# Kernel optimization log

Measured on AMD Instinct MI355X. Metric: run time of the kernel, lower is better.

Reference implementation:

```python
import jax, jax.numpy as jnp
import numpy as np

IN_N, OUT_N, KER, FEAT, HID = 50, 10, 10, 66, 256
VLEN = KER + OUT_N            # 20
VSEQ = IN_N - KER - OUT_N + 1 # 31
IF = 2 * VLEN                 # 40, GCN input feature size
NBLK = 12                     # 6 GC blocks x 2 graph convs
BN_EPS = 1e-5


def get_dct_matrix(N):
    k = np.arange(N)[:, None]
    i = np.arange(N)[None, :]
    w = np.full((N, 1), np.sqrt(2.0 / N))
    w[0, 0] = np.sqrt(1.0 / N)
    dct = (w * np.cos(np.pi * (i + 0.5) * k / N)).astype(np.float32)
    idct = np.linalg.inv(dct).astype(np.float32)
    return jnp.array(dct), jnp.array(idct)


def conv1d(x, w, b):
    # x: [B, Cin, T], w: [Cout, Cin, K]
    y = jax.lax.conv_general_dilated(x, w, (1,), 'VALID',
                                     dimension_numbers=('NCH', 'OIH', 'NCH'))
    return y + b[None, :, None]


def _forward(x, q_w1, q_b1, q_w2, q_b2, k_w1, k_b1, k_w2, k_b2,
             gin_w, gin_att, gin_b, bn_in_g, bn_in_b,
             blk_w, blk_att, blk_b, blk_bn_g, blk_bn_b,
             gout_w, gout_att, gout_b):
    dct, idct = get_dct_matrix(VLEN)
    B = x.shape[0]
    x = x[:, :IN_N]
    # q/k conv nets (Conv1d k=6 -> ReLU -> Conv1d k=5 -> ReLU)
    qs = jnp.transpose(x[:, IN_N - OUT_N:], (0, 2, 1))   # [B, FEAT, OUT_N]
    ksrc = jnp.transpose(x[:, :IN_N - OUT_N], (0, 2, 1)) # [B, FEAT, IN_N-OUT_N]
    q = jax.nn.relu(conv1d(jax.nn.relu(conv1d(qs, q_w1, q_b1)), q_w2, q_b2))    # [B, HID, 1]
    k = jax.nn.relu(conv1d(jax.nn.relu(conv1d(ksrc, k_w1, k_b1)), k_w2, k_b2))  # [B, HID, VSEQ]
    scores = jnp.einsum('bhq,bhs->bqs', q, k)            # [B, 1, VSEQ]
    att = scores[:, 0, :] / jnp.sum(scores, axis=-1)     # sum-normalized, [B, VSEQ]
    # overlapping windowed value gather + DCT
    vidx = np.arange(VLEN)[None, :] + np.arange(VSEQ)[:, None]
    value_mat = x[:, vidx, :]                             # [B, VSEQ, VLEN, FEAT]
    value_dct = jnp.einsum('bslf,lm->bsfm', value_mat, dct)  # [B, VSEQ, FEAT, VLEN]
    vdct_r = value_dct.reshape(B, FEAT, VSEQ, VLEN)       # raw reshape, as in torch source
    att_final = jnp.einsum('bs,bfsl->bfl', att, vdct_r)   # [B, FEAT, VLEN]
    # padded query (last KER frames + OUT_N repeats of last frame) in DCT space
    pidx = np.concatenate([np.arange(IN_N - KER, IN_N), np.full(OUT_N, IN_N - 1)])
    padded_query = jnp.einsum('bfl,lm->bfm', jnp.transpose(x[:, pidx], (0, 2, 1)), dct)
    gcn_inp = jnp.concatenate([padded_query, att_final], axis=2)  # [B, FEAT, IF]

    def gc(h, w, a, b):  # graph conv with learnable adjacency over FEAT nodes
        return jnp.einsum('nm,bmf->bnf', a, h @ w) + b

    def bn(h, g, beta):  # eval-mode BatchNorm1d over flattened [FEAT*feat] dim
        hf = h.reshape(B, -1)
        return ((hf / jnp.sqrt(1.0 + BN_EPS)) * g + beta).reshape(h.shape)

    y = jnp.tanh(bn(gc(gcn_inp, gin_w, gin_att, gin_b), bn_in_g, bn_in_b))
    for i in range(0, NBLK, 2):
        res = y
        y = jnp.tanh(bn(gc(y, blk_w[i], blk_att[i], blk_b[i]), blk_bn_g[i], blk_bn_b[i]))
        y = jnp.tanh(bn(gc(y, blk_w[i + 1], blk_att[i + 1], blk_b[i + 1]), blk_bn_g[i + 1], blk_bn_b[i + 1]))
        y = y + res
    gcn_out = gc(y, gout_w, gout_att, gout_b) + gcn_inp   # [B, FEAT, IF]
    return jnp.einsum('bfl,lm->bfm', gcn_out[:, :, :VLEN], idct)  # [B, FEAT, VLEN]


def setup_inputs():
    key = jax.random.key(0)
    ks = jax.random.split(key, 12)
    B = 2048
    s = 0.05
    NN = FEAT * HID
    return {
        'x': jax.random.normal(ks[0], (B, IN_N, FEAT), jnp.float32),
        'q_w1': jax.random.normal(ks[1], (HID, FEAT, 6), jnp.float32) * s,
        'q_b1': jnp.zeros((HID,), jnp.float32),
        'q_w2': jax.random.normal(ks[2], (HID, HID, 5), jnp.float32) * s,
        'q_b2': jnp.zeros((HID,), jnp.float32),
        'k_w1': jax.random.normal(ks[3], (HID, FEAT, 6), jnp.float32) * s,
        'k_b1': jnp.zeros((HID,), jnp.float32),
        'k_w2': jax.random.normal(ks[4], (HID, HID, 5), jnp.float32) * s,
        'k_b2': jnp.zeros((HID,), jnp.float32),
        'gin_w': jax.random.normal(ks[5], (IF, HID), jnp.float32) * s,
        'gin_att': jax.random.normal(ks[6], (FEAT, FEAT), jnp.float32) * s,
        'gin_b': jnp.zeros((HID,), jnp.float32),
        'bn_in_g': jnp.ones((NN,), jnp.float32),
        'bn_in_b': jnp.zeros((NN,), jnp.float32),
        'blk_w': jax.random.normal(ks[7], (NBLK, HID, HID), jnp.float32) * s,
        'blk_att': jax.random.normal(ks[8], (NBLK, FEAT, FEAT), jnp.float32) * s,
        'blk_b': jnp.zeros((NBLK, HID), jnp.float32),
        'blk_bn_g': jnp.ones((NBLK, NN), jnp.float32),
        'blk_bn_b': jnp.zeros((NBLK, NN), jnp.float32),
        'gout_w': jax.random.normal(ks[9], (HID, IF), jnp.float32) * s,
        'gout_att': jax.random.normal(ks[10], (FEAT, FEAT), jnp.float32) * s,
        'gout_b': jnp.zeros((IF,), jnp.float32),
    }


def reference(x, q_w1, q_b1, q_w2, q_b2, k_w1, k_b1, k_w2, k_b2,
              gin_w, gin_att, gin_b, bn_in_g, bn_in_b,
              blk_w, blk_att, blk_b, blk_bn_g, blk_bn_b,
              gout_w, gout_att, gout_b):
    return _forward(x, q_w1, q_b1, q_w2, q_b2, k_w1, k_b1, k_w2, k_b2,
                    gin_w, gin_att, gin_b, bn_in_g, bn_in_b,
                    blk_w, blk_att, blk_b, blk_bn_g, blk_bn_b,
                    gout_w, gout_att, gout_b)
```

## Files before the change

### kernel.cpp

```cpp
#include <hip/hip_runtime.h>
#include <math.h>

typedef unsigned short u16;
typedef unsigned int u32;

#define FEATN 66
#define HIDN 256
#define NNDIM 16896
#define INVS 0.9999950000374998f
#ifndef M_PI
#define M_PI 3.14159265358979323846
#endif

typedef __attribute__((ext_vector_type(4))) float f32x4;
typedef __attribute__((ext_vector_type(2))) float f32x2;
typedef __attribute__((ext_vector_type(8))) short s16x8;

__device__ __forceinline__ u32 bf_rne(float x) {
    u32 i = __float_as_uint(x);
    return (i + 0x7fffu + ((i >> 16) & 1u)) >> 16;
}

__global__ void dct_kernel(float* __restrict__ dct) {
    int t = threadIdx.x;
    if (t < 400) {
        int k = t / 20, i = t % 20;
        double w = (k == 0) ? sqrt(1.0 / 20.0) : sqrt(2.0 / 20.0);
        dct[t] = (float)(w * cos(M_PI * (i + 0.5) * k / 20.0));
    }
}

__global__ __launch_bounds__(256) void pack_w_kernel(
    const float* __restrict__ blk_w, u16* __restrict__ wh, u16* __restrict__ wl) {
    int gid = blockIdx.x * 256 + threadIdx.x;
    if (gid >= 12 * 65536) return;
    int layer = gid >> 16, rmd = gid & 65535;
    int ks = rmd >> 13;
    int r2 = rmd & 8191;
    int ct = r2 >> 9;
    int r3 = r2 & 511;
    int lane = r3 >> 3, j = r3 & 7;
    int k = ks * 32 + (lane >> 4) * 8 + j;
    int n = ct * 16 + (lane & 15);
    float v = blk_w[(size_t)layer * 65536 + k * 256 + n];
    u32 rhi = bf_rne(v);
    float hif = __uint_as_float(rhi << 16);
    u32 rlo = bf_rne(v - hif);
    wh[gid] = (u16)rhi;
    wl[gid] = (u16)rlo;
}

__global__ __launch_bounds__(256) void pack_w2_kernel(
    const float* __restrict__ w2, u16* __restrict__ wh, u16* __restrict__ wl) {
    int gid = blockIdx.x * 256 + threadIdx.x;
    if (gid >= 40 * 16 * 512) return;
    int ks = gid >> 13;
    int r2 = gid & 8191;
    int ct = r2 >> 9;
    int r3 = r2 & 511;
    int lane = r3 >> 3, j = r3 & 7;
    int k = ks * 32 + (lane >> 4) * 8 + j;
    int n = ct * 16 + (lane & 15);
    int h = k & 255, t = k >> 8;
    float v = w2[(size_t)n * 1280 + h * 5 + t];
    u32 rhi = bf_rne(v);
    float hif = __uint_as_float(rhi << 16);
    u32 rlo = bf_rne(v - hif);
    wh[gid] = (u16)rhi;
    wl[gid] = (u16)rlo;
}

__global__ __launch_bounds__(256) void pack_w1_kernel(
    const float* __restrict__ w1, u16* __restrict__ wh, u16* __restrict__ wl) {
    int gid = blockIdx.x * 256 + threadIdx.x;
    if (gid >= 13 * 16 * 512) return;
    int ks = gid >> 13;
    int r2 = gid & 8191;
    int ct = r2 >> 9;
    int r3 = r2 & 511;
    int lane = r3 >> 3, j = r3 & 7;
    int k = ks * 32 + (lane >> 4) * 8 + j;
    int n = ct * 16 + (lane & 15);
    float v = 0.f;
    if (k < 396) {
        int f = k % 66, t = k / 66;
        v = w1[(size_t)n * 396 + f * 6 + t];
    }
    u32 rhi = bf_rne(v);
    float hif = __uint_as_float(rhi << 16);
    u32 rlo = bf_rne(v - hif);
    wh[gid] = (u16)rhi;
    wl[gid] = (u16)rlo;
}

__global__ __launch_bounds__(256) void pack_att_kernel(
    const float* __restrict__ blk_att, u16* __restrict__ ah, u16* __restrict__ al) {
    int gid = blockIdx.x * 256 + threadIdx.x;
    if (gid >= 12 * 7680) return;
    int layer = gid / 7680, rem = gid % 7680;
    int rt = rem / 1536, rem2 = rem % 1536;
    int ks = rem2 / 512, r3 = rem2 % 512;
    int lane = r3 >> 3, j = r3 & 7;
    int n = rt * 16 + (lane & 15);
    int k = ks * 32 + (lane >> 4) * 8 + j;
    float v = (n < 66 && k < 66) ? blk_att[(size_t)layer * 4356 + n * 66 + k] : 0.f;
    u32 rhi = bf_rne(v);
    float hif = __uint_as_float(rhi << 16);
    u32 rlo = bf_rne(v - hif);
    ah[gid] = (u16)rhi;
    al[gid] = (u16)rlo;
}

__global__ __launch_bounds__(256, 1) void conv1_mfma_kernel(
    const float* __restrict__ x,
    const u16* __restrict__ whq, const u16* __restrict__ wlq,
    const u16* __restrict__ whk, const u16* __restrict__ wlk,
    const float* __restrict__ bq, const float* __restrict__ bk,
    float* __restrict__ q1, float* __restrict__ k1, int Cc, int nbq) {
    __shared__ u16 Ah[64 * 136];
    __shared__ u16 Al[64 * 136];
    const int tid = threadIdx.x;
    const int lane = tid & 63, wid = tid >> 6;
    const int m = lane & 15, quad = lane >> 4;
    const bool isq = ((int)blockIdx.x < nbq);
    const int bid = isq ? (int)blockIdx.x : ((int)blockIdx.x - nbq);
    const int rows = isq ? Cc * 5 : Cc * 35;
    const int row0 = bid * 64;
    const u16* wh = isq ? whq : whk;
    const u16* wl = isq ? wlq : wlk;
    const float* bias = isq ? bq : bk;
    float* out = isq ? q1 : k1;

    const int cq = tid & 31;
    const int r0t = (tid >> 5) * 8;
    int rbc[8]; bool vld[8];
#pragma unroll
    for (int s = 0; s < 8; s++) {
        int grow = row0 + r0t + s;
        int rbv;
        if (isq) { int bb = grow / 5;  rbv = bb * 3300 + 2640 + (grow - bb * 5) * 66; }
        else     { int bb = grow / 35; rbv = bb * 3300 + (grow - bb * 35) * 66; }
        vld[s] = (grow < rows);
        rbc[s] = vld[s] ? rbv : 0;
    }

    f32x4 acc[4][4];
#pragma unroll
    for (int rt = 0; rt < 4; rt++)
#pragma unroll
        for (int ct = 0; ct < 4; ct++) acc[rt][ct] = (f32x4)0.f;

    f32x2 ldA[16], ldB[16];

    auto LOADP = [&](f32x2* dst, int ph) {
        const int off = ph * 128 + cq * 4;
        const bool kok = (off < 396);
        const int o = kok ? off : 0;
#pragma unroll
        for (int s = 0; s < 8; s++) {
            const float* p = x + rbc[s] + o;
            dst[2 * s]     = *(const f32x2*)p;
            dst[2 * s + 1] = *(const f32x2*)(p + 2);
        }
    };
    auto STOREP = [&](const f32x2* src, int ph) {
        const bool kok = (ph * 128 + cq * 4) < 396;
#pragma unroll
        for (int s = 0; s < 8; s++) {
            float v0 = src[2 * s][0], v1 = src[2 * s][1];
            float v2 = src[2 * s + 1][0], v3 = src[2 * s + 1][1];
            if (!vld[s] || !kok) { v0 = v1 = v2 = v3 = 0.f; }
            u32 H0 = bf_rne(v0), H1 = bf_rne(v1), H2 = bf_rne(v2), H3 = bf_rne(v3);
            u32 L0 = bf_rne(v0 - __uint_as_float(H0 << 16));
            u32 L1 = bf_rne(v1 - __uint_as_float(H1 << 16));
            u32 L2 = bf_rne(v2 - __uint_as_float(H2 << 16));
            u32 L3 = bf_rne(v3 - __uint_as_float(H3 << 16));
            int o = (r0t + s) * 136 + cq * 4;
            *(uint2*)&Ah[o] = make_uint2(H0 | (H1 << 16), H2 | (H3 << 16));
            *(uint2*)&Al[o] = make_uint2(L0 | (L1 << 16), L2 | (L3 << 16));
        }
    };
    auto MFMAP = [&](int ph) {
#pragma unroll
        for (int ks = 0; ks < 4; ks++) {
            const int ksg = ph * 4 + ks;
            if (ksg >= 13) break;
            s16x8 ahf[4], alf[4], bhf[4], blf[4];
#pragma unroll
            for (int rt = 0; rt < 4; rt++) {
                int o2 = (rt * 16 + m) * 136 + ks * 32 + quad * 8;
                ahf[rt] = *(const s16x8*)&Ah[o2];
                alf[rt] = *(const s16x8*)&Al[o2];
            }
#pragma unroll
            for (int ct = 0; ct < 4; ct++) {
                size_t boff = ((size_t)(ksg * 16 + wid * 4 + ct)) * 512 + lane * 8;
                bhf[ct] = *(const s16x8*)&wh[boff];
                blf[ct] = *(const s16x8*)&wl[boff];
            }
#pragma unroll
            for (int rt = 0; rt < 4; rt++) {
#pragma unroll
                for (int ct = 0; ct < 4; ct++) {
                    acc[rt][ct] = __builtin_amdgcn_mfma_f32_16x16x32_bf16(
                        ahf[rt], bhf[ct], acc[rt][ct], 0, 0, 0);
                    acc[rt][ct] = __builtin_amdgcn_mfma_f32_16x16x32_bf16(
                        ahf[rt], blf[ct], acc[rt][ct], 0, 0, 0);
                    acc[rt][ct] = __builtin_amdgcn_mfma_f32_16x16x32_bf16(
                        alf[rt], bhf[ct], acc[rt][ct], 0, 0, 0);
                }
            }
        }
    };

    LOADP(ldA, 0);
    for (int ph = 0; ph < 4; ph += 2) {
        __syncthreads();
        STOREP(ldA, ph);
        LOADP(ldB, ph + 1);
        __syncthreads();
        MFMAP(ph);
        __syncthreads();
        STOREP(ldB, ph + 1);
        if (ph + 2 < 4) LOADP(ldA, ph + 2);
        __syncthreads();
        MFMAP(ph + 1);
    }

#pragma unroll
    for (int rt = 0; rt < 4; rt++) {
        int rb2 = row0 + rt * 16 + quad * 4;
#pragma unroll
        for (int r = 0; r < 4; r++) {
            int grow = rb2 + r;
            if (grow >= rows) continue;
#pragma unroll
            for (int ct = 0; ct < 4; ct++) {
                int f = wid * 64 + ct * 16 + m;
                float v = acc[rt][ct][r] + bias[f];
                out[(size_t)grow * 256 + f] = fmaxf(v, 0.f);
            }
        }
    }
}

__global__ __launch_bounds__(256, 1) void conv2_mfma_kernel(
    const float* __restrict__ Aq, const float* __restrict__ Ak,
    const u16* __restrict__ whq, const u16* __restrict__ wlq,
    const u16* __restrict__ whk, const u16* __restrict__ wlk,
    const float* __restrict__ bq, const float* __restrict__ bk,
    float* __restrict__ q2, float* __restrict__ k2, int Cc, int nbq) {
    __shared__ u16 Ah[64 * 136];
    __shared__ u16 Al[64 * 136];
    const int tid = threadIdx.x;
    const int lane = tid & 63, wid = tid >> 6;
    const int m = lane & 15, quad = lane >> 4;
    const bool isq = ((int)blockIdx.x < nbq);
    const int bid = isq ? (int)blockIdx.x : ((int)blockIdx.x - nbq);
    const int rows = isq ? Cc : Cc * 31;
    const int row0 = bid * 64;
    const float* Asrc = isq ? Aq : Ak;
    const u16* wh = isq ? whq : whk;
    const u16* wl = isq ? wlq : wlk;
    const float* bias = isq ? bq : bk;
    float* out = isq ? q2 : k2;

    const int cq = tid & 31;
    const int r0t = (tid >> 5) * 8;
    int rbc[8]; bool vld[8];
#pragma unroll
    for (int s = 0; s < 8; s++) {
        int grow = row0 + r0t + s;
        int rbv;
        if (isq) rbv = grow * 1280;
        else { int bb = grow / 31; rbv = bb * 8960 + (grow - bb * 31) * 256; }
        vld[s] = (grow < rows);
        rbc[s] = vld[s] ? rbv : 0;
    }

    f32x4 acc[4][4];
#pragma unroll
    for (int rt = 0; rt < 4; rt++)
#pragma unroll
        for (int ct = 0; ct < 4; ct++) acc[rt][ct] = (f32x4)0.f;

    f32x4 ldA[8], ldB[8];

    auto LOADP = [&](f32x4* dst, int ph) {
        const int off = ph * 128 + cq * 4;
#pragma unroll
        for (int s = 0; s < 8; s++)
            dst[s] = *(const f32x4*)(Asrc + rbc[s] + off);
    };
    auto STOREP = [&](const f32x4* src) {
#pragma unroll
        for (int s = 0; s < 8; s++) {
            f32x4 v = src[s];
            if (!vld[s]) v = (f32x4)0.f;
            u32 H0 = bf_rne(v[0]), H1 = bf_rne(v[1]), H2 = bf_rne(v[2]), H3 = bf_rne(v[3]);
            u32 L0 = bf_rne(v[0] - __uint_as_float(H0 << 16));
            u32 L1 = bf_rne(v[1] - __uint_as_float(H1 << 16));
            u32 L2 = bf_rne(v[2] - __uint_as_float(H2 << 16));
            u32 L3 = bf_rne(v[3] - __uint_as_float(H3 << 16));
            int o = (r0t + s) * 136 + cq * 4;
            *(uint2*)&Ah[o] = make_uint2(H0 | (H1 << 16), H2 | (H3 << 16));
            *(uint2*)&Al[o] = make_uint2(L0 | (L1 << 16), L2 | (L3 << 16));
        }
    };
    auto MFMAP = [&](int ph) {
#pragma unroll
        for (int ks = 0; ks < 4; ks++) {
            const int ksg = ph * 4 + ks;
            s16x8 ahf[4], alf[4], bhf[4], blf[4];
#pragma unroll
            for (int rt = 0; rt < 4; rt++) {
                int o2 = (rt * 16 + m) * 136 + ks * 32 + quad * 8;
                ahf[rt] = *(const s16x8*)&Ah[o2];
                alf[rt] = *(const s16x8*)&Al[o2];
            }
#pragma unroll
            for (int ct = 0; ct < 4; ct++) {
                size_t boff = ((size_t)(ksg * 16 + wid * 4 + ct)) * 512 + lane * 8;
                bhf[ct] = *(const s16x8*)&wh[boff];
                blf[ct] = *(const s16x8*)&wl[boff];
            }
#pragma unroll
            for (int rt = 0; rt < 4; rt++) {
#pragma unroll
                for (int ct = 0; ct < 4; ct++) {
                    acc[rt][ct] = __builtin_amdgcn_mfma_f32_16x16x32_bf16(
                        ahf[rt], bhf[ct], acc[rt][ct], 0, 0, 0);
                    acc[rt][ct] = __builtin_amdgcn_mfma_f32_16x16x32_bf16(
                        ahf[rt], blf[ct], acc[rt][ct], 0, 0, 0);
                    acc[rt][ct] = __builtin_amdgcn_mfma_f32_16x16x32_bf16(
                        alf[rt], bhf[ct], acc[rt][ct], 0, 0, 0);
                }
            }
        }
    };

    LOADP(ldA, 0);
    for (int ph = 0; ph < 10; ph += 2) {
        __syncthreads();
        STOREP(ldA);
        LOADP(ldB, ph + 1);
        __syncthreads();
        MFMAP(ph);
        __syncthreads();
        STOREP(ldB);
        if (ph + 2 < 10) LOADP(ldA, ph + 2);
        __syncthreads();
        MFMAP(ph + 1);
    }

#pragma unroll
    for (int rt = 0; rt < 4; rt++) {
        int rb2 = row0 + rt * 16 + quad * 4;
#pragma unroll
        for (int r = 0; r < 4; r++) {
            int grow = rb2 + r;
            if (grow >= rows) continue;
#pragma unroll
            for (int ct = 0; ct < 4; ct++) {
                int f = wid * 64 + ct * 16 + m;
                float v = acc[rt][ct][r] + bias[f];
                out[(size_t)grow * 256 + f] = fmaxf(v, 0.f);
            }
        }
    }
}

__global__ void att_kernel(const float* __restrict__ q2, const float* __restrict__ k2,
                           float* __restrict__ att) {
    __shared__ float q2s[256];
    const int b = blockIdx.x, tid = threadIdx.x;
    for (int i = tid; i < 256; i += 64) q2s[i] = q2[(size_t)b * 256 + i];
    __syncthreads();
    float sc = 0.f;
    if (tid < 31) {
        const f32x4* kp = (const f32x4*)(k2 + (size_t)b * 7936 + tid * 256);
        for (int c = 0; c < 64; c++) {
            f32x4 kv = kp[c];
            sc = fmaf(q2s[c * 4 + 0], kv[0], sc);
            sc = fmaf(q2s[c * 4 + 1], kv[1], sc);
            sc = fmaf(q2s[c * 4 + 2], kv[2], sc);
            sc = fmaf(q2s[c * 4 + 3], kv[3], sc);
        }
    }
    float tot = sc;
#pragma unroll
    for (int off = 1; off < 64; off <<= 1) tot += __shfl_xor(tot, off);
    if (tid < 31) att[(size_t)b * 32 + tid] = (tot != 0.f) ? (sc / tot) : 0.f;
}

__global__ __launch_bounds__(256) void gcn_inp_kernel(
    const float* __restrict__ x, const float* __restrict__ att,
    const float* __restrict__ dct, float* __restrict__ ginp) {
    __shared__ float xs[3300];
    __shared__ float dctS[400];
    __shared__ float attS[31];
    const int b = blockIdx.x, tid = threadIdx.x;
    const float* xb = x + (size_t)b * 3300;
    for (int idx = tid; idx < 3300; idx += 256) xs[idx] = xb[idx];
    for (int idx = tid; idx < 400; idx += 256) dctS[idx] = dct[idx];
    if (tid < 31) attS[tid] = att[(size_t)b * 32 + tid];
    __syncthreads();
    for (int idx = tid; idx < 2640; idx += 256) {
        int n = idx / 40, l = idx - n * 40;
        float acc = 0.f;
        if (l < 20) {
#pragma unroll
            for (int l1 = 0; l1 < 20; l1++) {
                int r = (l1 < 10) ? (40 + l1) : 49;
                acc = fmaf(xs[r * FEATN + n], dctS[l1 * 20 + l], acc);
            }
        } else {
            int j = l - 20;
            for (int s2 = 0; s2 < 31; s2++) {
                int mx = n * 31 + s2;
                int s1 = mx / 66, f1 = mx - s1 * 66;
                float inner = 0.f;
#pragma unroll
                for (int l1 = 0; l1 < 20; l1++)
                    inner = fmaf(xs[(s1 + l1) * FEATN + f1], dctS[l1 * 20 + j], inner);
                acc = fmaf(attS[s2], inner, acc);
            }
        }
        ginp[(size_t)b * 2640 + idx] = acc;
    }
}

__global__ __launch_bounds__(256) void attmul_gin_kernel(
    const float* __restrict__ ginp, const float* __restrict__ attm,
    float* __restrict__ out) {
    __shared__ float gS[2640];
    __shared__ float attS[4356];
    const int b = blockIdx.x, tid = threadIdx.x;
    for (int idx = tid; idx < 2640; idx += 256) gS[idx] = ginp[(size_t)b * 2640 + idx];
    for (int idx = tid; idx < 4356; idx += 256) attS[idx] = attm[idx];
    __syncthreads();
    for (int idx = tid; idx < 2640; idx += 256) {
        int n = idx / 40, l = idx - n * 40;
        float acc = 0.f;
        for (int mm = 0; mm < 66; mm++)
            acc = fmaf(attS[n * 66 + mm], gS[mm * 40 + l], acc);
        out[(size_t)b * 2640 + idx] = acc;
    }
}

__global__ __launch_bounds__(256) void attmul_kernel(
    const float* __restrict__ S, const float* __restrict__ attm,
    float* __restrict__ out) {
    __shared__ float Ss[66 * 64];
    __shared__ float attS[4356];
    const int b = blockIdx.x, tid = threadIdx.x;
    for (int idx = tid; idx < 4356; idx += 256) attS[idx] = attm[idx];
    const float* Sb = S + (size_t)b * NNDIM;
    float* ob = out + (size_t)b * NNDIM;
    const int fl = tid & 63, ng = tid >> 6;
    for (int f0 = 0; f0 < 256; f0 += 64) {
        __syncthreads();
        for (int idx = tid; idx < 66 * 64; idx += 256) {
            int mm = idx >> 6, j = idx & 63;
            Ss[idx] = Sb[mm * 256 + f0 + j];
        }
        __syncthreads();
        for (int n = ng; n < 66; n += 4) {
            float acc = 0.f;
            const float* ar = &attS[n * 66];
#pragma unroll 11
            for (int mm = 0; mm < 66; mm++)
                acc = fmaf(ar[mm], Ss[(mm << 6) + fl], acc);
            ob[n * 256 + f0 + fl] = acc;
        }
    }
}

template <int K, bool RES>
__global__ __launch_bounds__(256) void wmul_kernel(
    const float* __restrict__ Z, const float* __restrict__ W,
    const float* __restrict__ bias, const float* __restrict__ g,
    const float* __restrict__ beta, const float* __restrict__ res,
    float* __restrict__ out, int rows) {
    __shared__ float As[32 * K];
    const int tid = threadIdx.x;
    const size_t row0 = (size_t)blockIdx.x * 32;
    for (int idx = tid; idx < 32 * K; idx += 256) {
        int r = (int)row0 + idx / K;
        As[idx] = (r < rows) ? Z[row0 * K + idx] : 0.f;
    }
    __syncthreads();
    const int fq = tid & 63, rg = tid >> 6;
    float acc[8][4];
#pragma unroll
    for (int r = 0; r < 8; r++)
#pragma unroll
        for (int c = 0; c < 4; c++) acc[r][c] = 0.f;
    for (int i = 0; i < K; i += 4) {
        float w0[4], w1[4], w2[4], w3[4];
#pragma unroll
        for (int fi = 0; fi < 4; fi++) {
            w0[fi] = W[(size_t)(i + 0) * HIDN + fi * 64 + fq];
            w1[fi] = W[(size_t)(i + 1) * HIDN + fi * 64 + fq];
            w2[fi] = W[(size_t)(i + 2) * HIDN + fi * 64 + fq];
            w3[fi] = W[(size_t)(i + 3) * HIDN + fi * 64 + fq];
        }
#pragma unroll
        for (int rr = 0; rr < 8; rr++) {
            const float4 a = *(const float4*)&As[(rg * 8 + rr) * K + i];
#pragma unroll
            for (int fi = 0; fi < 4; fi++) {
                acc[rr][fi] = fmaf(a.x, w0[fi], acc[rr][fi]);
                acc[rr][fi] = fmaf(a.y, w1[fi], acc[rr][fi]);
                acc[rr][fi] = fmaf(a.z, w2[fi], acc[rr][fi]);
                acc[rr][fi] = fmaf(a.w, w3[fi], acc[rr][fi]);
            }
        }
    }
#pragma unroll
    for (int rr = 0; rr < 8; rr++) {
        int r = (int)row0 + rg * 8 + rr;
        if (r >= rows) continue;
        int n = r % 66;
#pragma unroll
        for (int fi = 0; fi < 4; fi++) {
            int f = fi * 64 + fq;
            float v = (acc[rr][fi] + bias[f]) * INVS;
            v = tanhf(fmaf(v, g[n * 256 + f], beta[n * 256 + f]));
            if (RES) v += res[(size_t)r * 256 + f];
            out[(size_t)r * 256 + f] = v;
        }
    }
}

__global__ __launch_bounds__(1024, 4) void trunk_kernel(
    float* __restrict__ Y,
    const u16* __restrict__ wpk_hi, const u16* __restrict__ wpk_lo,
    const u16* __restrict__ atA_hi, const u16* __restrict__ atA_lo,
    const float* __restrict__ blk_b,
    const float* __restrict__ bn_g, const float* __restrict__ bn_b) {
    __shared__ u16 Ainh[80 * 264];
    __shared__ u16 Ainl[80 * 264];
    __shared__ u16 Ubh[16 * 64 * 8];
    __shared__ u16 Ubl[16 * 64 * 8];
    const int tid = threadIdx.x;
    const int lane = tid & 63, wv = tid >> 6;
    const int m = lane & 15, quad = lane >> 4;
    const int b = blockIdx.x;
    float* Yb = Y + (size_t)b * NNDIM;
    const int f = wv * 16 + m;

    for (int idx = tid; idx < 8448; idx += 1024) {
        int r = idx >> 7, c2 = (idx & 127) * 2;
        float2 yv = *(const float2*)&Yb[r * 256 + c2];
        u32 h0 = bf_rne(yv.x), h1 = bf_rne(yv.y);
        u32 l0 = bf_rne(yv.x - __uint_as_float(h0 << 16));
        u32 l1 = bf_rne(yv.y - __uint_as_float(h1 << 16));
        *(u32*)&Ainh[r * 264 + c2] = h0 | (h1 << 16);
        *(u32*)&Ainl[r * 264 + c2] = l0 | (l1 << 16);
    }
    for (int idx = tid; idx < 14 * 264; idx += 1024) {
        Ainh[66 * 264 + idx] = 0; Ainl[66 * 264 + idx] = 0;
    }
    for (int idx = tid; idx < 8192; idx += 1024) { Ubh[idx] = 0; Ubl[idx] = 0; }

    float carry[5][4];
#pragma unroll
    for (int rt = 0; rt < 5; rt++)
#pragma unroll
        for (int r = 0; r < 4; r++) {
            int n = rt * 16 + quad * 4 + r;
            carry[rt][r] = (n < 66) ? Yb[n * 256 + f] : 0.f;
        }
    __syncthreads();

    for (int L = 0; L < 12; L++) {
        const u16* wh  = wpk_hi + (size_t)L * 65536;
        const u16* wl  = wpk_lo + (size_t)L * 65536;
        const u16* ath = atA_hi + (size_t)L * 7680;
        const u16* atl = atA_lo + (size_t)L * 7680;
        const float* bias = blk_b + (size_t)L * 256;
        const float* g    = bn_g + (size_t)L * NNDIM;
        const float* beta = bn_b + (size_t)L * NNDIM;
        const bool RES = (L & 1);

        f32x4 acc[5];
#pragma unroll
        for (int rt = 0; rt < 5; rt++) acc[rt] = (f32x4)0.f;

        s16x8 pbh = *(const s16x8*)&wh[(size_t)wv * 512 + lane * 8];
        s16x8 pbl = *(const s16x8*)&wl[(size_t)wv * 512 + lane * 8];
#pragma unroll
        for (int ks = 0; ks < 8; ks++) {
            s16x8 nbh, nbl;
            if (ks < 7) {
                size_t boff = ((size_t)((ks + 1) * 16 + wv)) * 512 + lane * 8;
                nbh = *(const s16x8*)&wh[boff];
                nbl = *(const s16x8*)&wl[boff];
            }
#pragma unroll
            for (int rt = 0; rt < 5; rt++) {
                int o2 = (rt * 16 + m) * 264 + ks * 32 + quad * 8;
                s16x8 ahf = *(const s16x8*)&Ainh[o2];
                s16x8 alf = *(const s16x8*)&Ainl[o2];
                acc[rt] = __builtin_amdgcn_mfma_f32_16x16x32_bf16(ahf, pbh, acc[rt], 0, 0, 0);
                acc[rt] = __builtin_amdgcn_mfma_f32_16x16x32_bf16(ahf, pbl, acc[rt], 0, 0, 0);
                acc[rt] = __builtin_amdgcn_mfma_f32_16x16x32_bf16(alf, pbh, acc[rt], 0, 0, 0);
            }
            if (ks < 7) { pbh = nbh; pbl = nbl; }
        }

        f32x4 acc2[5];
#pragma unroll
        for (int rt = 0; rt < 5; rt++) acc2[rt] = (f32x4)0.f;

#pragma unroll
        for (int ksf = 0; ksf < 3; ksf++) {
#pragma unroll
            for (int rr = 0; rr < 2; rr++) {
                const int rt = ksf * 2 + rr;
                if (rt > 4) continue;
                const int R0 = rt * 16 + quad * 4;
                const int quadf = (R0 >> 3) & 3;
                const int jb = R0 & 7;
                const int base = (wv * 64 + quadf * 16 + m) * 8 + jb;
                float v0 = acc[rt][0], v1 = acc[rt][1];
                float v2 = acc[rt][2], v3 = acc[rt][3];
                u32 H0 = bf_rne(v0), H1 = bf_rne(v1), H2 = bf_rne(v2), H3 = bf_rne(v3);
                u32 L0 = bf_rne(v0 - __uint_as_float(H0 << 16));
                u32 L1 = bf_rne(v1 - __uint_as_float(H1 << 16));
                u32 L2 = bf_rne(v2 - __uint_as_float(H2 << 16));
                u32 L3 = bf_rne(v3 - __uint_as_float(H3 << 16));
                *(uint2*)&Ubh[base] = make_uint2(H0 | (H1 << 16), H2 | (H3 << 16));
                *(uint2*)&Ubl[base] = make_uint2(L0 | (L1 << 16), L2 | (L3 << 16));
            }
            s16x8 ubh = *(const s16x8*)&Ubh[(wv * 64 + lane) * 8];
            s16x8 ubl = *(const s16x8*)&Ubl[(wv * 64 + lane) * 8];
#pragma unroll
            for (int rt = 0; rt < 5; rt++) {
                size_t aoff = ((size_t)(rt * 3 + ksf)) * 512 + lane * 8;
                s16x8 afh = *(const s16x8*)&ath[aoff];
                s16x8 afl = *(const s16x8*)&atl[aoff];
                acc2[rt] = __builtin_amdgcn_mfma_f32_16x16x32_bf16(afh, ubh, acc2[rt], 0, 0, 0);
                acc2[rt] = __builtin_amdgcn_mfma_f32_16x16x32_bf16(afh, ubl, acc2[rt], 0, 0, 0);
                acc2[rt] = __builtin_amdgcn_mfma_f32_16x16x32_bf16(afl, ubh, acc2[rt], 0, 0, 0);
            }
        }

        __syncthreads();
#pragma unroll
        for (int rt = 0; rt < 5; rt++) {
            const int nb = rt * 16 + quad * 4;
#pragma unroll
            for (int r = 0; r < 4; r++) {
                const int n = nb + r;
                if (n >= 66) continue;
                float v = (acc2[rt][r] + bias[f]) * INVS;
                v = tanhf(fmaf(v, g[n * 256 + f], beta[n * 256 + f]));
                if (RES) { v += carry[rt][r]; carry[rt][r] = v; }
                u32 H = bf_rne(v);
                u32 Lo = bf_rne(v - __uint_as_float(H << 16));
                Ainh[n * 264 + f] = (u16)H;
                Ainl[n * 264 + f] = (u16)Lo;
                if (L == 11) Yb[n * 256 + f] = v;
            }
        }
        __syncthreads();
    }
}

__global__ __launch_bounds__(256) void final_kernel(
    const float* __restrict__ T, const float* __restrict__ gw,
    const float* __restrict__ gb, const float* __restrict__ gi,
    const float* __restrict__ dct, float* __restrict__ out) {
    __shared__ float Zt[66 * 64];
    __shared__ float gwS[256 * 20];
    __shared__ float goS[1320];
    __shared__ float dctS[400];
    const int b = blockIdx.x, tid = threadIdx.x;
    for (int idx = tid; idx < 5120; idx += 256) {
        int i = idx / 20, l = idx - i * 20;
        gwS[idx] = gw[i * 40 + l];
    }
    for (int idx = tid; idx < 400; idx += 256) dctS[idx] = dct[idx];
    for (int idx = tid; idx < 1320; idx += 256) {
        int n = idx / 20, l = idx - n * 20;
        goS[idx] = gb[l] + gi[(size_t)b * 2640 + n * 40 + l];
    }
    for (int t = 0; t < 4; t++) {
        __syncthreads();
        for (int idx = tid; idx < 66 * 64; idx += 256) {
            int mm = idx >> 6, j = idx & 63;
            Zt[idx] = T[(size_t)b * NNDIM + mm * 256 + t * 64 + j];
        }
        __syncthreads();
        for (int idx = tid; idx < 1320; idx += 256) {
            int n = idx / 20, l = idx - n * 20;
            float acc = 0.f;
#pragma unroll
            for (int j = 0; j < 64; j++)
                acc = fmaf(Zt[(n << 6) + j], gwS[(t * 64 + j) * 20 + l], acc);
            goS[idx] += acc;
        }
    }
    __syncthreads();
    for (int idx = tid; idx < 1320; idx += 256) {
        int n = idx / 20, mm = idx - n * 20;
        float o = 0.f;
#pragma unroll
        for (int l = 0; l < 20; l++)
            o = fmaf(goS[n * 20 + l], dctS[mm * 20 + l], o);
        out[(size_t)b * 1320 + idx] = o;
    }
}

extern "C" void kernel_launch(void* const* d_in, const int* in_sizes, int n_in,
                              void* d_out, int out_size, void* d_ws, size_t ws_size,
                              hipStream_t stream) {
    const float* x        = (const float*)d_in[0];
    const float* q_w1     = (const float*)d_in[1];
    const float* q_b1     = (const float*)d_in[2];
    const float* q_w2     = (const float*)d_in[3];
    const float* q_b2     = (const float*)d_in[4];
    const float* k_w1     = (const float*)d_in[5];
    const float* k_b1     = (const float*)d_in[6];
    const float* k_w2     = (const float*)d_in[7];
    const float* k_b2     = (const float*)d_in[8];
    const float* gin_w    = (const float*)d_in[9];
    const float* gin_att  = (const float*)d_in[10];
    const float* gin_b    = (const float*)d_in[11];
    const float* bn_in_g  = (const float*)d_in[12];
    const float* bn_in_b  = (const float*)d_in[13];
    const float* blk_w    = (const float*)d_in[14];
    const float* blk_att  = (const float*)d_in[15];
    const float* blk_b    = (const float*)d_in[16];
    const float* blk_bn_g = (const float*)d_in[17];
    const float* blk_bn_b = (const float*)d_in[18];
    const float* gout_w   = (const float*)d_in[19];
    const float* gout_att = (const float*)d_in[20];
    const float* gout_b   = (const float*)d_in[21];
    float* out = (float*)d_out;

    const int B = in_sizes[0] / 3300;

    float* dctb = (float*)d_ws;
    u16* wpk_hi = (u16*)((char*)d_ws + 4096);
    u16* wpk_lo = wpk_hi + 12 * 65536;
    u16* w2q_hi = wpk_lo + 12 * 65536;
    u16* w2q_lo = w2q_hi + 40 * 16 * 512;
    u16* w2k_hi = w2q_lo + 40 * 16 * 512;
    u16* w2k_lo = w2k_hi + 40 * 16 * 512;
    u16* atA_hi = w2k_lo + 40 * 16 * 512;
    u16* atA_lo = atA_hi + 12 * 7680;
    u16* w1q_hi = atA_lo + 12 * 7680;
    u16* w1q_lo = w1q_hi + 13 * 16 * 512;
    u16* w1k_hi = w1q_lo + 13 * 16 * 512;
    u16* w1k_lo = w1k_hi + 13 * 16 * 512;
    const size_t BASE = 4096 + (size_t)2 * 12 * 65536 * 2 + (size_t)4 * 40 * 16 * 512 * 2
                        + (size_t)2 * 12 * 7680 * 2 + (size_t)4 * 13 * 16 * 512 * 2;
    char* R = (char*)d_ws + BASE;
    size_t avail = (ws_size > BASE) ? (ws_size - BASE) : 0;

    const size_t PER_B = 36720ull * 4ull;
    int C = B;
    while (C > 1 && (size_t)C * PER_B > avail) C >>= 1;

    dct_kernel<<<1, 512, 0, stream>>>(dctb);
    pack_w_kernel<<<(12 * 65536) / 256, 256, 0, stream>>>(blk_w, wpk_hi, wpk_lo);
    pack_w2_kernel<<<(40 * 16 * 512) / 256, 256, 0, stream>>>(q_w2, w2q_hi, w2q_lo);
    pack_w2_kernel<<<(40 * 16 * 512) / 256, 256, 0, stream>>>(k_w2, w2k_hi, w2k_lo);
    pack_att_kernel<<<(12 * 7680) / 256, 256, 0, stream>>>(blk_att, atA_hi, atA_lo);
    pack_w1_kernel<<<(13 * 16 * 512) / 256, 256, 0, stream>>>(q_w1, w1q_hi, w1q_lo);
    pack_w1_kernel<<<(13 * 16 * 512) / 256, 256, 0, stream>>>(k_w1, w1k_hi, w1k_lo);

    for (int c0 = 0; c0 < B; c0 += C) {
        const int Cc = (B - c0 < C) ? (B - c0) : C;
        const float* xc = x + (size_t)c0 * 3300;
        float* outc = out + (size_t)c0 * 1320;

        float* Yb  = (float*)R;
        float* Tb  = Yb + (size_t)C * 16896;
        float* gib = Tb + (size_t)C * 16896;
        float* ab  = gib + (size_t)C * 2640;
        float* q2b = ab + (size_t)C * 32;
        float* k1b = Yb;
        float* k2b = Tb;
        float* q1b = gib;

        const int c1q = (Cc * 5 + 63) / 64, c1k = (Cc * 35 + 63) / 64;
        conv1_mfma_kernel<<<c1q + c1k, 256, 0, stream>>>(
            xc, w1q_hi, w1q_lo, w1k_hi, w1k_lo, q_b1, k_b1, q1b, k1b, Cc, c1q);
        const int c2q = (Cc + 63) / 64, c2k = (Cc * 31 + 63) / 64;
        conv2_mfma_kernel<<<c2q + c2k, 256, 0, stream>>>(
            q1b, k1b, w2q_hi, w2q_lo, w2k_hi, w2k_lo, q_b2, k_b2, q2b, k2b, Cc, c2q);
        att_kernel<<<Cc, 64, 0, stream>>>(q2b, k2b, ab);
        gcn_inp_kernel<<<Cc, 256, 0, stream>>>(xc, ab, dctb, gib);

        const int rows = Cc * FEATN;
        const int g32 = (rows + 31) / 32;

        attmul_gin_kernel<<<Cc, 256, 0, stream>>>(gib, gin_att, Tb);
        wmul_kernel<40, false><<<g32, 256, 0, stream>>>(Tb, gin_w, gin_b,
                                                        bn_in_g, bn_in_b, nullptr, Yb, rows);
        trunk_kernel<<<Cc, 1024, 0, stream>>>(Yb, wpk_hi, wpk_lo, atA_hi, atA_lo,
                                              blk_b, blk_bn_g, blk_bn_b);
        attmul_kernel<<<Cc, 256, 0, stream>>>(Yb, gout_att, Tb);
        final_kernel<<<Cc, 256, 0, stream>>>(Tb, gout_w, gout_b, gib, dctb, outc);
    }
}
```

Before: 4.564 ms.

## Halve trunk kernel block to 512 threads with two column tiles per wave

The trunk kernel now launches 512 threads per batch element and each wave handles two 16-column output tiles instead of one. LDS A-fragments read per k-step are reused across both column tiles, which halves shared-memory traffic per MFMA. The cost is doubled accumulator and carry registers per thread, with the launch bound changed to (512,1). Fewer waves per block may reduce latency hiding.

```diff
diff --git a/kernel.cpp b/kernel.cpp
--- a/kernel.cpp
+++ b/kernel.cpp
@@ -533,7 +533,7 @@
     }
 }
 
-__global__ __launch_bounds__(1024, 4) void trunk_kernel(
+__global__ __launch_bounds__(512, 1) void trunk_kernel(
     float* __restrict__ Y,
     const u16* __restrict__ wpk_hi, const u16* __restrict__ wpk_lo,
     const u16* __restrict__ atA_hi, const u16* __restrict__ atA_lo,
@@ -548,9 +548,9 @@
     const int m = lane & 15, quad = lane >> 4;
     const int b = blockIdx.x;
     float* Yb = Y + (size_t)b * NNDIM;
-    const int f = wv * 16 + m;
-
-    for (int idx = tid; idx < 8448; idx += 1024) {
+    const int fc[2] = { (wv * 2 + 0) * 16 + m, (wv * 2 + 1) * 16 + m };
+
+    for (int idx = tid; idx < 8448; idx += 512) {
         int r = idx >> 7, c2 = (idx & 127) * 2;
         float2 yv = *(const float2*)&Yb[r * 256 + c2];
         u32 h0 = bf_rne(yv.x), h1 = bf_rne(yv.y);
@@ -559,18 +559,20 @@
         *(u32*)&Ainh[r * 264 + c2] = h0 | (h1 << 16);
         *(u32*)&Ainl[r * 264 + c2] = l0 | (l1 << 16);
     }
-    for (int idx = tid; idx < 14 * 264; idx += 1024) {
+    for (int idx = tid; idx < 14 * 264; idx += 512) {
         Ainh[66 * 264 + idx] = 0; Ainl[66 * 264 + idx] = 0;
     }
-    for (int idx = tid; idx < 8192; idx += 1024) { Ubh[idx] = 0; Ubl[idx] = 0; }
-
-    float carry[5][4];
+    for (int idx = tid; idx < 8192; idx += 512) { Ubh[idx] = 0; Ubl[idx] = 0; }
+
+    float carry[5][4][2];
 #pragma unroll
     for (int rt = 0; rt < 5; rt++)
 #pragma unroll
         for (int r = 0; r < 4; r++) {
             int n = rt * 16 + quad * 4 + r;
-            carry[rt][r] = (n < 66) ? Yb[n * 256 + f] : 0.f;
+#pragma unroll
+            for (int ci = 0; ci < 2; ci++)
+                carry[rt][r][ci] = (n < 66) ? Yb[n * 256 + fc[ci]] : 0.f;
         }
     __syncthreads();
 
@@ -584,35 +586,56 @@
         const float* beta = bn_b + (size_t)L * NNDIM;
         const bool RES = (L & 1);
 
-        f32x4 acc[5];
-#pragma unroll
-        for (int rt = 0; rt < 5; rt++) acc[rt] = (f32x4)0.f;
-
-        s16x8 pbh = *(const s16x8*)&wh[(size_t)wv * 512 + lane * 8];
-        s16x8 pbl = *(const s16x8*)&wl[(size_t)wv * 512 + lane * 8];
+        f32x4 acc[5][2];
+#pragma unroll
+        for (int rt = 0; rt < 5; rt++)
+#pragma unroll
+            for (int ci = 0; ci < 2; ci++) acc[rt][ci] = (f32x4)0.f;
+
+        s16x8 pbh[2], pbl[2];
+#pragma unroll
+        for (int ci = 0; ci < 2; ci++) {
+            size_t boff = ((size_t)(wv * 2 + ci)) * 512 + lane * 8;
+            pbh[ci] = *(const s16x8*)&wh[boff];
+            pbl[ci] = *(const s16x8*)&wl[boff];
+        }
 #pragma unroll
         for (int ks = 0; ks < 8; ks++) {
-            s16x8 nbh, nbl;
+            s16x8 nbh[2], nbl[2];
             if (ks < 7) {
-                size_t boff = ((size_t)((ks + 1) * 16 + wv)) * 512 + lane * 8;
-                nbh = *(const s16x8*)&wh[boff];
-                nbl = *(const s16x8*)&wl[boff];
+#pragma unroll
+                for (int ci = 0; ci < 2; ci++) {
+                    size_t boff = ((size_t)((ks + 1) * 16 + wv * 2 + ci)) * 512 + lane * 8;
+                    nbh[ci] = *(const s16x8*)&wh[boff];
+                    nbl[ci] = *(const s16x8*)&wl[boff];
+                }
             }
 #pragma unroll
             for (int rt = 0; rt < 5; rt++) {
                 int o2 = (rt * 16 + m) * 264 + ks * 32 + quad * 8;
                 s16x8 ahf = *(const s16x8*)&Ainh[o2];
                 s16x8 alf = *(const s16x8*)&Ainl[o2];
-                acc[rt] = __builtin_amdgcn_mfma_f32_16x16x32_bf16(ahf, pbh, acc[rt], 0, 0, 0);
-                acc[rt] = __builtin_amdgcn_mfma_f32_16x16x32_bf16(ahf, pbl, acc[rt], 0, 0, 0);
-                acc[rt] = __builtin_amdgcn_mfma_f32_16x16x32_bf16(alf, pbh, acc[rt], 0, 0, 0);
-            }
-            if (ks < 7) { pbh = nbh; pbl = nbl; }
-        }
-
-        f32x4 acc2[5];
-#pragma unroll
-        for (int rt = 0; rt < 5; rt++) acc2[rt] = (f32x4)0.f;
+#pragma unroll
+                for (int ci = 0; ci < 2; ci++) {
+                    acc[rt][ci] = __builtin_amdgcn_mfma_f32_16x16x32_bf16(
+                        ahf, pbh[ci], acc[rt][ci], 0, 0, 0);
+                    acc[rt][ci] = __builtin_amdgcn_mfma_f32_16x16x32_bf16(
+                        ahf, pbl[ci], acc[rt][ci], 0, 0, 0);
+                    acc[rt][ci] = __builtin_amdgcn_mfma_f32_16x16x32_bf16(
+                        alf, pbh[ci], acc[rt][ci], 0, 0, 0);
+                }
+            }
+            if (ks < 7) {
+#pragma unroll
+                for (int ci = 0; ci < 2; ci++) { pbh[ci] = nbh[ci]; pbl[ci] = nbl[ci]; }
+            }
+        }
+
+        f32x4 acc2[5][2];
+#pragma unroll
+        for (int rt = 0; rt < 5; rt++)
+#pragma unroll
+            for (int ci = 0; ci < 2; ci++) acc2[rt][ci] = (f32x4)0.f;
 
 #pragma unroll
         for (int ksf = 0; ksf < 3; ksf++) {
@@ -623,27 +646,42 @@
                 const int R0 = rt * 16 + quad * 4;
                 const int quadf = (R0 >> 3) & 3;
                 const int jb = R0 & 7;
-                const int base = (wv * 64 + quadf * 16 + m) * 8 + jb;
-                float v0 = acc[rt][0], v1 = acc[rt][1];
-                float v2 = acc[rt][2], v3 = acc[rt][3];
-                u32 H0 = bf_rne(v0), H1 = bf_rne(v1), H2 = bf_rne(v2), H3 = bf_rne(v3);
-                u32 L0 = bf_rne(v0 - __uint_as_float(H0 << 16));
-                u32 L1 = bf_rne(v1 - __uint_as_float(H1 << 16));
-                u32 L2 = bf_rne(v2 - __uint_as_float(H2 << 16));
-                u32 L3 = bf_rne(v3 - __uint_as_float(H3 << 16));
-                *(uint2*)&Ubh[base] = make_uint2(H0 | (H1 << 16), H2 | (H3 << 16));
-                *(uint2*)&Ubl[base] = make_uint2(L0 | (L1 << 16), L2 | (L3 << 16));
-            }
-            s16x8 ubh = *(const s16x8*)&Ubh[(wv * 64 + lane) * 8];
-            s16x8 ubl = *(const s16x8*)&Ubl[(wv * 64 + lane) * 8];
+#pragma unroll
+                for (int ci = 0; ci < 2; ci++) {
+                    const int ctg = wv * 2 + ci;
+                    const int base = (ctg * 64 + quadf * 16 + m) * 8 + jb;
+                    float v0 = acc[rt][ci][0], v1 = acc[rt][ci][1];
+                    float v2 = acc[rt][ci][2], v3 = acc[rt][ci][3];
+                    u32 H0 = bf_rne(v0), H1 = bf_rne(v1), H2 = bf_rne(v2), H3 = bf_rne(v3);
+                    u32 L0 = bf_rne(v0 - __uint_as_float(H0 << 16));
+                    u32 L1 = bf_rne(v1 - __uint_as_float(H1 << 16));
+                    u32 L2 = bf_rne(v2 - __uint_as_float(H2 << 16));
+                    u32 L3 = bf_rne(v3 - __uint_as_float(H3 << 16));
+                    *(uint2*)&Ubh[base] = make_uint2(H0 | (H1 << 16), H2 | (H3 << 16));
+                    *(uint2*)&Ubl[base] = make_uint2(L0 | (L1 << 16), L2 | (L3 << 16));
+                }
+            }
+            s16x8 ubh[2], ubl[2];
+#pragma unroll
+            for (int ci = 0; ci < 2; ci++) {
+                int uoff = ((wv * 2 + ci) * 64 + lane) * 8;
+                ubh[ci] = *(const s16x8*)&Ubh[uoff];
+                ubl[ci] = *(const s16x8*)&Ubl[uoff];
+            }
 #pragma unroll
             for (int rt = 0; rt < 5; rt++) {
                 size_t aoff = ((size_t)(rt * 3 + ksf)) * 512 + lane * 8;
                 s16x8 afh = *(const s16x8*)&ath[aoff];
                 s16x8 afl = *(const s16x8*)&atl[aoff];
-                acc2[rt] = __builtin_amdgcn_mfma_f32_16x16x32_bf16(afh, ubh, acc2[rt], 0, 0, 0);
-                acc2[rt] = __builtin_amdgcn_mfma_f32_16x16x32_bf16(afh, ubl, acc2[rt], 0, 0, 0);
-                acc2[rt] = __builtin_amdgcn_mfma_f32_16x16x32_bf16(afl, ubh, acc2[rt], 0, 0, 0);
+#pragma unroll
+                for (int ci = 0; ci < 2; ci++) {
+                    acc2[rt][ci] = __builtin_amdgcn_mfma_f32_16x16x32_bf16(
+                        afh, ubh[ci], acc2[rt][ci], 0, 0, 0);
+                    acc2[rt][ci] = __builtin_amdgcn_mfma_f32_16x16x32_bf16(
+                        afh, ubl[ci], acc2[rt][ci], 0, 0, 0);
+                    acc2[rt][ci] = __builtin_amdgcn_mfma_f32_16x16x32_bf16(
+                        afl, ubh[ci], acc2[rt][ci], 0, 0, 0);
+                }
             }
         }
 
@@ -655,14 +693,18 @@
             for (int r = 0; r < 4; r++) {
                 const int n = nb + r;
                 if (n >= 66) continue;
-                float v = (acc2[rt][r] + bias[f]) * INVS;
-                v = tanhf(fmaf(v, g[n * 256 + f], beta[n * 256 + f]));
-                if (RES) { v += carry[rt][r]; carry[rt][r] = v; }
-                u32 H = bf_rne(v);
-                u32 Lo = bf_rne(v - __uint_as_float(H << 16));
-                Ainh[n * 264 + f] = (u16)H;
-                Ainl[n * 264 + f] = (u16)Lo;
-                if (L == 11) Yb[n * 256 + f] = v;
+#pragma unroll
+                for (int ci = 0; ci < 2; ci++) {
+                    const int f = fc[ci];
+                    float v = (acc2[rt][ci][r] + bias[f]) * INVS;
+                    v = tanhf(fmaf(v, g[n * 256 + f], beta[n * 256 + f]));
+                    if (RES) { v += carry[rt][r][ci]; carry[rt][r][ci] = v; }
+                    u32 H = bf_rne(v);
+                    u32 Lo = bf_rne(v - __uint_as_float(H << 16));
+                    Ainh[n * 264 + f] = (u16)H;
+                    Ainl[n * 264 + f] = (u16)Lo;
+                    if (L == 11) Yb[n * 256 + f] = v;
+                }
             }
         }
         __syncthreads();
@@ -802,8 +844,8 @@
         attmul_gin_kernel<<<Cc, 256, 0, stream>>>(gib, gin_att, Tb);
         wmul_kernel<40, false><<<g32, 256, 0, stream>>>(Tb, gin_w, gin_b,
                                                         bn_in_g, bn_in_b, nullptr, Yb, rows);
-        trunk_kernel<<<Cc, 1024, 0, stream>>>(Yb, wpk_hi, wpk_lo, atA_hi, atA_lo,
-                                              blk_b, blk_bn_g, blk_bn_b);
+        trunk_kernel<<<Cc, 512, 0, stream>>>(Yb, wpk_hi, wpk_lo, atA_hi, atA_lo,
+                                             blk_b, blk_bn_g, blk_bn_b);
         attmul_kernel<<<Cc, 256, 0, stream>>>(Yb, gout_att, Tb);
         final_kernel<<<Cc, 256, 0, stream>>>(Tb, gout_w, gout_b, gib, dctb, outc);
     }
```

New measurement: 5.390 ms. 1.18x slower.
